# Optimization experiments

Measured on AMD Instinct MI355X. Metric: run time of the kernel, lower is better.

Reference implementation:

```python
import jax, jax.numpy as jnp
import numpy as np

N = 50000
E = 800000
D = 128
O = 128


def _spmm_coo(rows, cols, vals, x, n_rows):
    # out[r] += vals[e] * x[cols[e]]  (COO sparse matrix times dense matrix)
    gathered = vals[:, None] * x[cols]            # [E, O]
    return jax.ops.segment_sum(gathered, rows, num_segments=n_rows)


def setup_inputs() -> dict:
    key = jax.random.key(0)
    ks = jax.random.split(key, 9)
    return {
        "inputs": jax.random.normal(ks[0], (N, D), dtype=jnp.float32),
        "adj1_rows": jax.random.randint(ks[1], (E,), 0, N, dtype=jnp.int32),
        "adj1_cols": jax.random.randint(ks[2], (E,), 0, N, dtype=jnp.int32),
        "adj1_vals": jax.random.uniform(ks[3], (E,), dtype=jnp.float32),
        "adj2_rows": jax.random.randint(ks[4], (E,), 0, N, dtype=jnp.int32),
        "adj2_cols": jax.random.randint(ks[5], (E,), 0, N, dtype=jnp.int32),
        "adj2_vals": jax.random.uniform(ks[6], (E,), dtype=jnp.float32),
        "weights_1": jax.random.normal(ks[7], (D, O), dtype=jnp.float32) * (6.0 / (D + O)) ** 0.5,
        "weights_2": jax.random.normal(ks[8], (D, O), dtype=jnp.float32) * (6.0 / (D + O)) ** 0.5,
    }


def reference(inputs, adj1_rows, adj1_cols, adj1_vals,
              adj2_rows, adj2_cols, adj2_vals, weights_1, weights_2):
    # dense projection per relation
    x1 = inputs @ weights_1                        # [N, O]
    x2 = inputs @ weights_2                        # [N, O]
    # sparse aggregation per relation
    y1 = _spmm_coo(adj1_rows, adj1_cols, adj1_vals, x1, N)
    y2 = _spmm_coo(adj2_rows, adj2_cols, adj2_vals, x2, N)
    return jax.nn.relu(y1 + y2)
```

## Files before the change

### kernel.cpp

```cpp
#include <hip/hip_runtime.h>


typedef __attribute__((ext_vector_type(4))) float     f32x4;
typedef __attribute__((ext_vector_type(8))) short     bf16x8;

#define NB      782
#define BSLOTS  10
#define BCAP    2560
#define CAPH    1536

static __device__ __forceinline__ unsigned short f2bf(float f) {
    unsigned u = __float_as_uint(f);
    u += 0x7FFF + ((u >> 16) & 1);
    return (unsigned short)(u >> 16);
}

__global__ __launch_bounds__(256) void convert_kernel(
    const float* __restrict__ X,
    const float* __restrict__ W1, const float* __restrict__ W2,
    unsigned short* __restrict__ Xb, unsigned short* __restrict__ Wt, int n)
{
    const int stride = gridDim.x * blockDim.x;
    const int nW = 2 * 128 * 128;
    const int nX = n * 32;
    const int total = nW + nX;
    for (int g = blockIdx.x * blockDim.x + threadIdx.x; g < total; g += stride) {
        if (g < nW) {
            const int rel = g >> 14;
            const int o   = (g >> 7) & 127;
            const int k   = g & 127;
            const float* W = rel ? W2 : W1;
            Wt[g] = f2bf(W[k * 128 + o]);
        } else {
            const int i = g - nW;
            const float4 v = ((const float4*)X)[i];
            ushort4 b;
            b.x = f2bf(v.x); b.y = f2bf(v.y); b.z = f2bf(v.z); b.w = f2bf(v.w);
            ((ushort4*)Xb)[i] = b;
        }
    }
}

__global__ __launch_bounds__(256) void bin_kernel(
    const int* __restrict__ rows1, const int* __restrict__ cols1, const float* __restrict__ vals1,
    const int* __restrict__ rows2, const int* __restrict__ cols2, const float* __restrict__ vals2,
    int* __restrict__ gcur, unsigned long long* __restrict__ edges_tmp,
    int E, int n)
{
    __shared__ unsigned long long stage[NB][BSLOTS];
    __shared__ int scnt[NB];

    for (int i = threadIdx.x; i < NB; i += 256) scnt[i] = 0;
    __syncthreads();

    const int stride = gridDim.x * 256;
    const int total  = 2 * E;
    for (int g = blockIdx.x * 256 + threadIdx.x; g < total; g += stride) {
        int r, col, rel; float v;
        if (g < E) { r = rows1[g]; col = cols1[g]; rel = 0; v = vals1[g]; }
        else       { int e = g - E; r = rows2[e]; col = cols2[e]; rel = 1; v = vals2[e]; }

        const int b = r >> 6;
        const unsigned lo = (unsigned)(r & 63) | ((unsigned)rel << 6) | ((unsigned)col << 7);
        const unsigned long long pack =
            (unsigned long long)lo | ((unsigned long long)__float_as_uint(v) << 32);

        const int pos = atomicAdd(&scnt[b], 1);
        if (pos < BSLOTS) {
            stage[b][pos] = pack;
        } else {
            int gp = atomicAdd(&gcur[b], 1);
            if (gp < BCAP) edges_tmp[(size_t)b * BCAP + gp] = pack;
        }
    }
    __syncthreads();

    for (int b = threadIdx.x; b < NB; b += 256) {
        int k = scnt[b]; if (k > BSLOTS) k = BSLOTS;
        if (k > 0) {
            int base = atomicAdd(&gcur[b], k);
            for (int i = 0; i < k; ++i)
                if (base + i < BCAP)
                    edges_tmp[(size_t)b * BCAP + base + i] = stage[b][i];
        }
    }
}

__global__ __launch_bounds__(256) void agg_kernel(
    const int* __restrict__ gcur,
    const unsigned long long* __restrict__ edges_tmp,
    const unsigned short* __restrict__ Xb,
    unsigned short* __restrict__ agg, int n)
{
    __shared__ unsigned long long csr[CAPH];
    __shared__ int cnt[64];
    __shared__ int ptr[65];
    __shared__ int cur[64];

    const int nwg = NB * 2;
    const int xcd = blockIdx.x & 7, bi = blockIdx.x >> 3;
    const int q8 = nwg >> 3, r8 = nwg & 7;
    const int swz = (xcd < r8) ? xcd * (q8 + 1) + bi
                               : r8 * (q8 + 1) + (xcd - r8) * q8 + bi;

    const int b   = swz >> 1;
    const int h   = swz & 1;
    const int tid = threadIdx.x;
    const int rowbase = b * 64 + h * 32;
    if (rowbase >= n) return;

    int sz = gcur[b]; if (sz > BCAP) sz = BCAP;
    const unsigned long long* ebase = edges_tmp + (size_t)b * BCAP;

    if (tid < 64) cnt[tid] = 0;
    __syncthreads();

    for (int e = tid; e < sz; e += 256) {
        const unsigned lo = (unsigned)ebase[e];
        const int rl = (int)(lo & 63u);
        if ((rl >> 5) == h) atomicAdd(&cnt[((rl & 31) << 1) | ((lo >> 6) & 1)], 1);
    }
    __syncthreads();

    if (tid < 64) {
        const int v = cnt[tid];
        int x = v;
        #pragma unroll
        for (int off = 1; off < 64; off <<= 1) {
            int t = __shfl_up(x, off, 64);
            if (tid >= off) x += t;
        }
        ptr[tid + 1] = x;
        cur[tid]     = x - v;
    }
    if (tid == 0) ptr[0] = 0;
    __syncthreads();

    for (int e = tid; e < sz; e += 256) {
        const unsigned long long p = ebase[e];
        const unsigned lo = (unsigned)p;
        const int rl = (int)(lo & 63u);
        if ((rl >> 5) == h) {
            const int pos = atomicAdd(&cur[((rl & 31) << 1) | ((lo >> 6) & 1)], 1);
            if (pos < CAPH) csr[pos] = p;
        }
    }
    __syncthreads();

    const int lane = tid & 31;
    const int grp  = tid >> 5;
    for (int seg = grp; seg < 64; seg += 8) {
        const int row = rowbase + (seg >> 1);
        if (row >= n) continue;
        const int rel = seg & 1;
        const int s  = ptr[seg];
        const int e2 = ptr[seg + 1];
        float4 acc = make_float4(0.f, 0.f, 0.f, 0.f);

        int e = s;
        for (; e + 4 <= e2; e += 4) {
            const unsigned long long p0 = csr[e + 0];
            const unsigned long long p1 = csr[e + 1];
            const unsigned long long p2 = csr[e + 2];
            const unsigned long long p3 = csr[e + 3];
            const ushort4 x0 = *(const ushort4*)&Xb[(size_t)(((unsigned)p0 >> 7) & 0xFFFFu) * 128 + lane * 4];
            const ushort4 x1 = *(const ushort4*)&Xb[(size_t)(((unsigned)p1 >> 7) & 0xFFFFu) * 128 + lane * 4];
            const ushort4 x2 = *(const ushort4*)&Xb[(size_t)(((unsigned)p2 >> 7) & 0xFFFFu) * 128 + lane * 4];
            const ushort4 x3 = *(const ushort4*)&Xb[(size_t)(((unsigned)p3 >> 7) & 0xFFFFu) * 128 + lane * 4];
            const float v0 = __uint_as_float((unsigned)(p0 >> 32));
            const float v1 = __uint_as_float((unsigned)(p1 >> 32));
            const float v2 = __uint_as_float((unsigned)(p2 >> 32));
            const float v3 = __uint_as_float((unsigned)(p3 >> 32));
            acc.x = fmaf(v0, __uint_as_float((unsigned)x0.x << 16), acc.x);
            acc.y = fmaf(v0, __uint_as_float((unsigned)x0.y << 16), acc.y);
            acc.z = fmaf(v0, __uint_as_float((unsigned)x0.z << 16), acc.z);
            acc.w = fmaf(v0, __uint_as_float((unsigned)x0.w << 16), acc.w);
            acc.x = fmaf(v1, __uint_as_float((unsigned)x1.x << 16), acc.x);
            acc.y = fmaf(v1, __uint_as_float((unsigned)x1.y << 16), acc.y);
            acc.z = fmaf(v1, __uint_as_float((unsigned)x1.z << 16), acc.z);
            acc.w = fmaf(v1, __uint_as_float((unsigned)x1.w << 16), acc.w);
            acc.x = fmaf(v2, __uint_as_float((unsigned)x2.x << 16), acc.x);
            acc.y = fmaf(v2, __uint_as_float((unsigned)x2.y << 16), acc.y);
            acc.z = fmaf(v2, __uint_as_float((unsigned)x2.z << 16), acc.z);
            acc.w = fmaf(v2, __uint_as_float((unsigned)x2.w << 16), acc.w);
            acc.x = fmaf(v3, __uint_as_float((unsigned)x3.x << 16), acc.x);
            acc.y = fmaf(v3, __uint_as_float((unsigned)x3.y << 16), acc.y);
            acc.z = fmaf(v3, __uint_as_float((unsigned)x3.z << 16), acc.z);
            acc.w = fmaf(v3, __uint_as_float((unsigned)x3.w << 16), acc.w);
        }
        for (; e < e2; ++e) {
            const unsigned long long p = csr[e];
            const ushort4 xv = *(const ushort4*)&Xb[(size_t)(((unsigned)p >> 7) & 0xFFFFu) * 128 + lane * 4];
            const float v  = __uint_as_float((unsigned)(p >> 32));
            acc.x = fmaf(v, __uint_as_float((unsigned)xv.x << 16), acc.x);
            acc.y = fmaf(v, __uint_as_float((unsigned)xv.y << 16), acc.y);
            acc.z = fmaf(v, __uint_as_float((unsigned)xv.z << 16), acc.z);
            acc.w = fmaf(v, __uint_as_float((unsigned)xv.w << 16), acc.w);
        }

        ushort4 o;
        o.x = f2bf(acc.x); o.y = f2bf(acc.y); o.z = f2bf(acc.z); o.w = f2bf(acc.w);
        *(ushort4*)&agg[((size_t)rel * n + row) * 128 + lane * 4] = o;
    }
}

__global__ __launch_bounds__(256) void gemm_relu_kernel(
    const unsigned short* __restrict__ agg,
    const unsigned short* __restrict__ Wt,
    float* __restrict__ out, int n)
{
    const int lane = threadIdx.x & 63;
    const int w    = threadIdx.x >> 6;
    const int colbase = w * 32;
    const int l15 = lane & 15;
    const int lhi = lane >> 4;

    bf16x8 bfrag[2][2][4];
    #pragma unroll
    for (int rel = 0; rel < 2; ++rel) {
        const unsigned short* Wr = Wt + rel * 16384;
        #pragma unroll
        for (int ct = 0; ct < 2; ++ct) {
            const int o = colbase + ct * 16 + l15;
            #pragma unroll
            for (int ks = 0; ks < 4; ++ks)
                bfrag[rel][ct][ks] = *(const bf16x8*)&Wr[o * 128 + ks * 32 + lhi * 8];
        }
    }

    const int row0 = blockIdx.x * 64;
    const f32x4 zero = {0.f, 0.f, 0.f, 0.f};

    #pragma unroll
    for (int rt = 0; rt < 4; ++rt) {
        const int r0 = row0 + rt * 16;
        int ra = r0 + l15; if (ra >= n) ra = n - 1;
        bf16x8 af0[4], af1[4];
        #pragma unroll
        for (int ks = 0; ks < 4; ++ks) {
            af0[ks] = *(const bf16x8*)&agg[(size_t)ra * 128 + ks * 32 + lhi * 8];
            af1[ks] = *(const bf16x8*)&agg[((size_t)n + ra) * 128 + ks * 32 + lhi * 8];
        }

        f32x4 acc[2];
        acc[0] = zero; acc[1] = zero;
        #pragma unroll
        for (int ks = 0; ks < 4; ++ks) {
            acc[0] = __builtin_amdgcn_mfma_f32_16x16x32_bf16(af0[ks], bfrag[0][0][ks], acc[0], 0, 0, 0);
            acc[1] = __builtin_amdgcn_mfma_f32_16x16x32_bf16(af0[ks], bfrag[0][1][ks], acc[1], 0, 0, 0);
            acc[0] = __builtin_amdgcn_mfma_f32_16x16x32_bf16(af1[ks], bfrag[1][0][ks], acc[0], 0, 0, 0);
            acc[1] = __builtin_amdgcn_mfma_f32_16x16x32_bf16(af1[ks], bfrag[1][1][ks], acc[1], 0, 0, 0);
        }

        #pragma unroll
        for (int ct = 0; ct < 2; ++ct) {
            const int col = colbase + ct * 16 + l15;
            #pragma unroll
            for (int j = 0; j < 4; ++j) {
                const int r = r0 + lhi * 4 + j;
                if (r < n) out[(size_t)r * 128 + col] = fmaxf(acc[ct][j], 0.f);
            }
        }
    }
}

extern "C" void kernel_launch(void* const* d_in, const int* in_sizes, int n_in,
                              void* d_out, int out_size, void* d_ws, size_t ws_size,
                              hipStream_t stream)
{
    const float* X  = (const float*)d_in[0];
    const int*   r1 = (const int*)  d_in[1];
    const int*   c1 = (const int*)  d_in[2];
    const float* v1 = (const float*)d_in[3];
    const int*   r2 = (const int*)  d_in[4];
    const int*   c2 = (const int*)  d_in[5];
    const float* v2 = (const float*)d_in[6];
    const float* W1 = (const float*)d_in[7];
    const float* W2 = (const float*)d_in[8];
    float*       out = (float*)d_out;

    const int n = in_sizes[0] / 128;
    const int E = in_sizes[1];

    unsigned short* agg = (unsigned short*)d_ws;
    unsigned short* Xb  = agg + (size_t)2 * n * 128;
    unsigned short* Wt  = Xb + (size_t)n * 128;
    unsigned long long* edges_tmp =
        (unsigned long long*)(((uintptr_t)(Wt + 2 * 128 * 128) + 255) & ~(uintptr_t)255);
    int* gcur = (int*)(edges_tmp + (size_t)NB * BCAP);

    hipMemsetAsync(gcur, 0, NB * sizeof(int), stream);

    convert_kernel<<<2048, 256, 0, stream>>>(X, W1, W2, Xb, Wt, n);

    bin_kernel<<<512, 256, 0, stream>>>(r1, c1, v1, r2, c2, v2, gcur, edges_tmp, E, n);

    agg_kernel<<<NB * 2, 256, 0, stream>>>(gcur, edges_tmp, Xb, agg, n);

    gemm_relu_kernel<<<(n + 63) / 64, 256, 0, stream>>>(agg, Wt, out, n);
}
```

Baseline: 129.6 us.

## Split aggregation into quarter-bin workgroups with fixed-capacity per-segment LDS lists

Each 64-row bin is now handled by four workgroups of 16 rows instead of two of 32. The count, scan and scatter passes that built a compact CSR in LDS are replaced by a single pass that atomically appends each edge into a fixed 64-slot list per (row, relation) segment. This removes one pass over the bin's edges and a barrier, and doubles the number of workgroups. In exchange, every workgroup re-reads the whole bin, so edge-list traffic doubles, and any segment with more than 64 edges is silently truncated. The GEMM kernel is also changed to 32 rows per block, doubling its grid.

```diff
diff --git a/kernel.cpp b/kernel.cpp
--- a/kernel.cpp
+++ b/kernel.cpp
@@ -7,7 +7,7 @@
 #define NB      782
 #define BSLOTS  10
 #define BCAP    2560
-#define CAPH    1536
+#define SCAP    64
 
 static __device__ __forceinline__ unsigned short f2bf(float f) {
     unsigned u = __float_as_uint(f);
@@ -92,77 +92,54 @@
     const unsigned short* __restrict__ Xb,
     unsigned short* __restrict__ agg, int n)
 {
-    __shared__ unsigned long long csr[CAPH];
-    __shared__ int cnt[64];
-    __shared__ int ptr[65];
-    __shared__ int cur[64];
-
-    const int nwg = NB * 2;
+    __shared__ unsigned long long lists[32 * SCAP];
+    __shared__ int cnt[32];
+
+    const int nwg = NB * 4;
     const int xcd = blockIdx.x & 7, bi = blockIdx.x >> 3;
-    const int q8 = nwg >> 3, r8 = nwg & 7;
-    const int swz = (xcd < r8) ? xcd * (q8 + 1) + bi
-                               : r8 * (q8 + 1) + (xcd - r8) * q8 + bi;
-
-    const int b   = swz >> 1;
-    const int h   = swz & 1;
+    const int q8 = nwg >> 3;
+    const int swz = xcd * q8 + bi;
+
+    const int b   = swz >> 2;
+    const int q   = swz & 3;
     const int tid = threadIdx.x;
-    const int rowbase = b * 64 + h * 32;
+    const int rowbase = b * 64 + q * 16;
     if (rowbase >= n) return;
 
     int sz = gcur[b]; if (sz > BCAP) sz = BCAP;
     const unsigned long long* ebase = edges_tmp + (size_t)b * BCAP;
 
-    if (tid < 64) cnt[tid] = 0;
-    __syncthreads();
-
-    for (int e = tid; e < sz; e += 256) {
-        const unsigned lo = (unsigned)ebase[e];
-        const int rl = (int)(lo & 63u);
-        if ((rl >> 5) == h) atomicAdd(&cnt[((rl & 31) << 1) | ((lo >> 6) & 1)], 1);
-    }
-    __syncthreads();
-
-    if (tid < 64) {
-        const int v = cnt[tid];
-        int x = v;
-        #pragma unroll
-        for (int off = 1; off < 64; off <<= 1) {
-            int t = __shfl_up(x, off, 64);
-            if (tid >= off) x += t;
-        }
-        ptr[tid + 1] = x;
-        cur[tid]     = x - v;
-    }
-    if (tid == 0) ptr[0] = 0;
+    if (tid < 32) cnt[tid] = 0;
     __syncthreads();
 
     for (int e = tid; e < sz; e += 256) {
         const unsigned long long p = ebase[e];
         const unsigned lo = (unsigned)p;
         const int rl = (int)(lo & 63u);
-        if ((rl >> 5) == h) {
-            const int pos = atomicAdd(&cur[((rl & 31) << 1) | ((lo >> 6) & 1)], 1);
-            if (pos < CAPH) csr[pos] = p;
+        if ((rl >> 4) == q) {
+            const int seg = ((rl & 15) << 1) | ((lo >> 6) & 1);
+            const int pos = atomicAdd(&cnt[seg], 1);
+            if (pos < SCAP) lists[seg * SCAP + pos] = p;
         }
     }
     __syncthreads();
 
     const int lane = tid & 31;
     const int grp  = tid >> 5;
-    for (int seg = grp; seg < 64; seg += 8) {
+    for (int seg = grp; seg < 32; seg += 8) {
         const int row = rowbase + (seg >> 1);
         if (row >= n) continue;
         const int rel = seg & 1;
-        const int s  = ptr[seg];
-        const int e2 = ptr[seg + 1];
+        int m = cnt[seg]; if (m > SCAP) m = SCAP;
+        const unsigned long long* lst = &lists[seg * SCAP];
         float4 acc = make_float4(0.f, 0.f, 0.f, 0.f);
 
-        int e = s;
-        for (; e + 4 <= e2; e += 4) {
-            const unsigned long long p0 = csr[e + 0];
-            const unsigned long long p1 = csr[e + 1];
-            const unsigned long long p2 = csr[e + 2];
-            const unsigned long long p3 = csr[e + 3];
+        int e = 0;
+        for (; e + 4 <= m; e += 4) {
+            const unsigned long long p0 = lst[e + 0];
+            const unsigned long long p1 = lst[e + 1];
+            const unsigned long long p2 = lst[e + 2];
+            const unsigned long long p3 = lst[e + 3];
             const ushort4 x0 = *(const ushort4*)&Xb[(size_t)(((unsigned)p0 >> 7) & 0xFFFFu) * 128 + lane * 4];
             const ushort4 x1 = *(const ushort4*)&Xb[(size_t)(((unsigned)p1 >> 7) & 0xFFFFu) * 128 + lane * 4];
             const ushort4 x2 = *(const ushort4*)&Xb[(size_t)(((unsigned)p2 >> 7) & 0xFFFFu) * 128 + lane * 4];
@@ -188,8 +165,8 @@
             acc.z = fmaf(v3, __uint_as_float((unsigned)x3.z << 16), acc.z);
             acc.w = fmaf(v3, __uint_as_float((unsigned)x3.w << 16), acc.w);
         }
-        for (; e < e2; ++e) {
-            const unsigned long long p = csr[e];
+        for (; e < m; ++e) {
+            const unsigned long long p = lst[e];
             const ushort4 xv = *(const ushort4*)&Xb[(size_t)(((unsigned)p >> 7) & 0xFFFFu) * 128 + lane * 4];
             const float v  = __uint_as_float((unsigned)(p >> 32));
             acc.x = fmaf(v, __uint_as_float((unsigned)xv.x << 16), acc.x);
@@ -228,11 +205,11 @@
         }
     }
 
-    const int row0 = blockIdx.x * 64;
+    const int row0 = blockIdx.x * 32;
     const f32x4 zero = {0.f, 0.f, 0.f, 0.f};
 
     #pragma unroll
-    for (int rt = 0; rt < 4; ++rt) {
+    for (int rt = 0; rt < 2; ++rt) {
         const int r0 = row0 + rt * 16;
         int ra = r0 + l15; if (ra >= n) ra = n - 1;
         bf16x8 af0[4], af1[4];
@@ -295,7 +272,7 @@
 
     bin_kernel<<<512, 256, 0, stream>>>(r1, c1, v1, r2, c2, v2, gcur, edges_tmp, E, n);
 
-    agg_kernel<<<NB * 2, 256, 0, stream>>>(gcur, edges_tmp, Xb, agg, n);
-
-    gemm_relu_kernel<<<(n + 63) / 64, 256, 0, stream>>>(agg, Wt, out, n);
-}
+    agg_kernel<<<NB * 4, 256, 0, stream>>>(gcur, edges_tmp, Xb, agg, n);
+
+    gemm_relu_kernel<<<(n + 31) / 32, 256, 0, stream>>>(agg, Wt, out, n);
+}
```

New measurement: 129.8 us. About the same (+0.1%).
